# Kernel tuning notes

Hardware: AMD Instinct MI355X
Metric: run time of the kernel (lower is better)

The kernel has to match this reference:

```python
import jax, jax.numpy as jnp
import numpy as np

_J6 = jnp.array([[0,0,0,0,0,1],[0,0,0,0,-1,0],[0,0,0,1,0,0],
                 [0,0,1,0,0,0],[0,-1,0,0,0,0],[1,0,0,0,0,0]], dtype=jnp.float32)
_PAIRS4 = [(0,1),(0,2),(0,3),(1,2),(1,3),(2,3)]  # combinations(range(4),2)


def exterior(p1, p2):
    # Plucker line coords of two 4-vectors, normalized. (...,4)x(...,4)->(...,6)
    parts = [p1[..., i] * p2[..., j] - p1[..., j] * p2[..., i] for i, j in _PAIRS4]
    L = jnp.stack(parts, axis=-1)
    n = jnp.maximum(jnp.linalg.norm(L, axis=-1, keepdims=True), 1e-12)
    return L / n


def setup_inputs() -> dict:
    key = jax.random.key(0)
    B, T, D, H = 2, 2048, 1024, 16
    ks = jax.random.split(key, 10)
    w = lambda k, shape: jax.random.normal(k, shape, jnp.float32) * 0.02
    return {
        "x": jax.random.normal(ks[0], (B, T, D), jnp.float32),
        "qkv_w": w(ks[1], (3 * D, D)),
        "qkv_b": jnp.zeros((3 * D,), jnp.float32),
        "w1w": w(ks[2], (4 * H, D)),
        "w2w": w(ks[3], (4 * H, D)),
        "r1w": w(ks[4], (4 * H, D)),
        "r2w": w(ks[5], (4 * H, D)),
        "memv_w": w(ks[6], (D, D)),
        "memv_b": jnp.zeros((D,), jnp.float32),
        "memg_w": w(ks[7], (H, D)),
        "memg_b": jnp.zeros((H,), jnp.float32),
        "mem_scale": jnp.full((H,), 0.1, jnp.float32),
        "iter_mix": jnp.array(0.0, jnp.float32),
        "out_w": w(ks[8], (D, D)),
        "out_b": jnp.zeros((D,), jnp.float32),
        "decay_logits": jnp.full((H,), 4.6, jnp.float32),
    }


def reference(x, qkv_w, qkv_b, w1w, w2w, r1w, r2w, memv_w, memv_b,
              memg_w, memg_b, mem_scale, iter_mix, out_w, out_b, decay_logits):
    B, T, D = x.shape
    H = decay_logits.shape[0]
    dh = D // H
    pd = 6
    scale = dh ** -0.5

    # --- standard causal softmax attention ---
    qkv = (x @ qkv_w.T + qkv_b).reshape(B, T, 3, H, dh)
    qkv = jnp.transpose(qkv, (2, 0, 3, 1, 4))  # (3,B,H,T,dh)
    q, k, v = qkv[0], qkv[1], qkv[2]
    scores = jnp.einsum('bhtd,bhsd->bhts', q, k) * scale
    causal = jnp.triu(jnp.ones((T, T), dtype=bool), 1)
    scores = jnp.where(causal, -jnp.inf, scores)
    attn = jax.nn.softmax(scores, axis=-1)  # dropout is identity in eval
    seq_out = jnp.einsum('bhts,bhsd->bhtd', attn, v)
    seq_out = jnp.transpose(seq_out, (0, 2, 1, 3)).reshape(B, T, D)

    # --- decay-weighted Gram memory (linear-attention style state) ---
    x_prev = jnp.concatenate([jnp.zeros((B, 1, D), x.dtype), x[:, :-1]], axis=1)
    w1 = (x_prev @ w1w.T).reshape(B, T, H, 4)
    w2 = (x @ w2w.T).reshape(B, T, H, 4)
    write_lines = exterior(w1, w2)  # (B,T,H,6)
    r1 = (x @ r1w.T).reshape(B, T, H, 4)
    r2 = (x @ r2w.T).reshape(B, T, H, 4)
    read_lines = exterior(r1, r2)

    Jw = jnp.einsum('bthi,ij->bhtj', write_lines, _J6)  # (B,H,T,6)
    rd = jnp.transpose(read_lines, (0, 2, 1, 3))        # (B,H,T,6)

    decays = jax.nn.sigmoid(decay_logits)               # (H,)
    pos = jnp.arange(T, dtype=x.dtype)
    outer = Jw[..., :, None] * Jw[..., None, :]         # (B,H,T,6,6)
    decay_inv = (1.0 / jnp.maximum(decays, 1e-6))[:, None] ** pos[None, :]  # (H,T)
    outer_scaled = outer * decay_inv[None, :, :, None, None]
    M_cumsum = jnp.cumsum(outer_scaled, axis=2)
    M_cumsum = jnp.concatenate(
        [jnp.zeros((B, H, 1, pd, pd), x.dtype), M_cumsum[:, :, :-1]], axis=2)
    decay_fwd = decays[:, None] ** pos[None, :]
    M_all = M_cumsum * decay_fwd[None, :, :, None, None]

    rd_M = jnp.einsum('bhti,bhtij->bhtj', rd, M_all)
    score_M = jnp.sum(rd_M * rd, axis=-1)    # (B,H,T)
    score_M2 = jnp.sum(rd_M * rd_M, axis=-1)
    alpha = jax.nn.sigmoid(iter_mix)
    mem_score = (1 - alpha) * score_M + alpha * score_M2

    mem_val = x @ memv_w.T + memv_b                     # (B,T,D)
    gate = jax.nn.sigmoid(x @ memg_w.T + memg_b)        # (B,T,H)
    mem_score_t = jnp.transpose(mem_score, (0, 2, 1))   # (B,T,H)
    gated = jax.nn.sigmoid(mem_score_t * mem_scale) * gate
    gated = jnp.mean(gated, axis=-1, keepdims=True)     # (B,T,1)

    return (seq_out + gated * mem_val) @ out_w.T + out_b
```

## Files before the change

kernel.cpp:

```cpp
#include <hip/hip_runtime.h>
#include <stdint.h>

#define TT 2048
#define DD 1024
#define HH 16
#define LDP 4368
#define SCH 64
#define SNC (TT/SCH)

using bf16x8 = __attribute__((ext_vector_type(8))) __bf16;
using u16x8  = __attribute__((ext_vector_type(8))) unsigned short;
using f32x4  = __attribute__((ext_vector_type(4))) float;

__device__ __forceinline__ float bf2f(unsigned short u){
  unsigned int x = ((unsigned int)u) << 16;
  return __builtin_bit_cast(float, x);
}
__device__ __forceinline__ unsigned short f2bf(float f){
  unsigned int x = __builtin_bit_cast(unsigned int, f);
  x += 0x7fffu + ((x >> 16) & 1u);
  return (unsigned short)(x >> 16);
}
__device__ __forceinline__ float sigmoidf_(float x){ return 1.0f/(1.0f+__expf(-x)); }

__device__ __forceinline__ void gload_lds16(const void* g, void* l){
  auto gp = (const __attribute__((address_space(1))) unsigned int*)(uintptr_t)g;
  auto lp = (__attribute__((address_space(3))) unsigned int*)(unsigned int)(uintptr_t)l;
  __builtin_amdgcn_global_load_lds(gp, lp, 16, 0, 0);
}

__global__ void prep_all_kernel(const float* __restrict__ qkv_w, const float* __restrict__ w1w,
                                const float* __restrict__ w2w, const float* __restrict__ r1w,
                                const float* __restrict__ r2w, const float* __restrict__ memv_w,
                                const float* __restrict__ memg_w, const float* __restrict__ out_w,
                                const float* __restrict__ qkv_b, const float* __restrict__ memv_b,
                                const float* __restrict__ memg_b, const float* __restrict__ x,
                                unsigned short* __restrict__ Wcat, float* __restrict__ bcat,
                                unsigned short* __restrict__ xb)
{
  const int blk = blockIdx.x;
  if (blk < 5392) {
    const int idx = blk*256 + threadIdx.x;
    {
      const int row = idx >> 8, c4 = (idx & 255)*4;
      const float* src; int r;
      if      (row < 3072) { src = qkv_w;  r = row; }
      else if (row < 3136) { src = w1w;    r = row-3072; }
      else if (row < 3200) { src = w2w;    r = row-3136; }
      else if (row < 3264) { src = r1w;    r = row-3200; }
      else if (row < 3328) { src = r2w;    r = row-3264; }
      else if (row < 4352) { src = memv_w; r = row-3328; }
      else if (row < 4368) { src = memg_w; r = row-4352; }
      else                 { src = out_w;  r = row-4368; }
      const float4 v = *(const float4*)(src + (size_t)r*1024 + c4);
      ushort4 o; o.x=f2bf(v.x); o.y=f2bf(v.y); o.z=f2bf(v.z); o.w=f2bf(v.w);
      *(ushort4*)(Wcat + (size_t)row*1024 + c4) = o;
    }
    if (idx < 4368) {
      float v;
      if      (idx < 3072) v = qkv_b[idx];
      else if (idx < 3328) v = 0.f;
      else if (idx < 4352) v = memv_b[idx-3328];
      else                 v = memg_b[idx-4352];
      bcat[idx] = v;
    }
  } else {
    const int idx = (blk - 5392)*256 + threadIdx.x;
    const float4 v = ((const float4*)x)[idx];
    ushort4 o; o.x=f2bf(v.x); o.y=f2bf(v.y); o.z=f2bf(v.z); o.w=f2bf(v.w);
    ((ushort4*)xb)[idx] = o;
  }
}

template<bool OUTF32>
__global__ __launch_bounds__(256, 3)
void gemm_bt_kernel(const unsigned short* __restrict__ A, int lda,
                    const unsigned short* __restrict__ Bt, int ldb,
                    const float* __restrict__ bias,
                    void* __restrict__ Cout, int ldc, int N, int K,
                    unsigned short* __restrict__ VTout)
{
  __shared__ unsigned short smem[24576];
  const int tid = threadIdx.x;
  const int w = tid >> 6, lane = tid & 63;
  const int l15 = lane & 15, l4 = lane >> 4;
  const int m0 = blockIdx.x * 128;
  const int n0 = blockIdx.y * 128;
  const int wr = (w >> 1) * 64, wc = (w & 1) * 64;

  const f32x4 zero = {0.f,0.f,0.f,0.f};
  f32x4 acc[4][4];
#pragma unroll
  for (int i = 0; i < 4; ++i)
#pragma unroll
    for (int j = 0; j < 4; ++j) acc[i][j] = zero;

  const int srow = lane >> 2;
  const int k8   = (lane & 3) * 8;

  auto stage = [&](int k0, int buf) {
#pragma unroll
    for (int q = 0; q < 4; ++q) {
      const int c = q*4 + w;
      const int rloc = (c & 7)*16 + srow;
      if (c < 8) {
        gload_lds16(A + (size_t)(m0 + rloc)*lda + k0 + k8,
                    (char*)smem + buf*8192 + (c&7)*1024);
      } else {
        int nrow = n0 + rloc; if (nrow >= N) nrow = N - 1;
        gload_lds16(Bt + (size_t)nrow*ldb + k0 + k8,
                    (char*)smem + 24576 + buf*8192 + (c&7)*1024);
      }
    }
  };

  stage(0, 0);
  if (K > 32) stage(32, 1);

  int ti = 0;
  for (int k0 = 0; k0 < K; k0 += 32, ++ti) {
    if (k0 + 32 < K) { asm volatile("s_waitcnt vmcnt(4)" ::: "memory"); }
    else             { asm volatile("s_waitcnt vmcnt(0)" ::: "memory"); }
    __builtin_amdgcn_s_barrier();
    if (k0 + 64 < K) stage(k0 + 64, (ti + 2) % 3);

    const int cur = ti % 3;
    bf16x8 af[4], bfr[4];
#pragma unroll
    for (int i = 0; i < 4; ++i) {
      af[i]  = *reinterpret_cast<const bf16x8*>((const char*)smem + cur*8192
                 + (wr + i*16 + l15)*64 + l4*16);
      bfr[i] = *reinterpret_cast<const bf16x8*>((const char*)smem + 24576 + cur*8192
                 + (wc + i*16 + l15)*64 + l4*16);
    }
#pragma unroll
    for (int i = 0; i < 4; ++i)
#pragma unroll
      for (int j = 0; j < 4; ++j)
        acc[i][j] = __builtin_amdgcn_mfma_f32_16x16x32_bf16(af[i], bfr[j], acc[i][j], 0, 0, 0);
  }

  if (OUTF32) {
#pragma unroll
    for (int i = 0; i < 4; ++i) {
      const int rowb = m0 + wr + i*16 + l4*4;
#pragma unroll
      for (int j = 0; j < 4; ++j) {
        const int col = n0 + wc + j*16 + l15;
        if (col < N) {
          const float bv = bias ? bias[col] : 0.0f;
#pragma unroll
          for (int r = 0; r < 4; ++r)
            ((float*)Cout)[(size_t)(rowb + r)*ldc + col] = acc[i][j][r] + bv;
        }
      }
    }
  } else {
    __syncthreads();
    const bool isV = (VTout != nullptr) && (n0 >= 2048) && (n0 < 3072);
#pragma unroll
    for (int i = 0; i < 4; ++i) {
      const int rloc = wr + i*16 + l4*4;
#pragma unroll
      for (int j = 0; j < 4; ++j) {
        const int col = wc + j*16 + l15;
        const float bv = bias ? bias[n0 + col] : 0.0f;
#pragma unroll
        for (int r = 0; r < 4; ++r) {
          const int row = rloc + r;
          const unsigned byte = (unsigned)row*256u
                              + (((unsigned)col*2u) ^ (((unsigned)row & 15u) << 4));
          *(unsigned short*)((char*)smem + byte) = f2bf(acc[i][j][r] + bv);
        }
      }
    }
    __syncthreads();
    if (!isV) {
#pragma unroll
      for (int p = 0; p < 8; ++p) {
        const int idx = p*256 + tid;
        const int row = idx >> 4;
        const int c8  = (idx & 15) * 8;
        if (n0 + c8 + 8 <= N) {
          const unsigned byte = (unsigned)row*256u
                              + (((unsigned)(c8*2)) ^ (((unsigned)row & 15u) << 4));
          *(u16x8*)((unsigned short*)Cout + (size_t)(m0 + row)*ldc + n0 + c8) =
              *(const u16x8*)((const char*)smem + byte);
        }
      }
    } else {
      const int vbase = ((m0 >> 11)*HH + ((n0 - 2048) >> 6)) * 64;
      const int t0 = m0 & (TT - 1);
      for (int it = 0; it < 64; ++it) {
        const int i2 = it*256 + tid;
        const int d2 = i2 >> 7;
        const int tl = i2 & 127;
        const unsigned byte = (unsigned)tl*256u
                            + (((unsigned)d2*2u) ^ (((unsigned)tl & 15u) << 4));
        VTout[(size_t)(vbase + d2)*TT + t0 + tl] =
            *(const unsigned short*)((const char*)smem + byte);
      }
    }
  }
}

__global__ __launch_bounds__(256, 2)
void attn_kernel(const unsigned short* __restrict__ P,
                 const unsigned short* __restrict__ VT,
                 float* __restrict__ seqo)
{
  __shared__ unsigned short Ks[2][128*64];
  __shared__ unsigned short Vs[2][64*128];
  __shared__ unsigned short Pls[4][16*128];

  const int tid = threadIdx.x;
  const int w = tid >> 6, lane = tid & 63;
  const int l15 = lane & 15, l4 = lane >> 4;

  const int n = blockIdx.x;
  const int xcd = n & 7, slot = n >> 3;
  const int grp = slot >> 4, pi = slot & 15;
  const int g = grp*8 + xcd;
  const int h = g & 15, b = g >> 4;

  auto stage = [&](int kt, int bufsel) {
#pragma unroll
    for (int q2 = 0; q2 < 4; ++q2) {
      const int idx = q2*256 + tid;
      {
        const int r = idx >> 3;
        const int cb = ((idx & 7)*16) ^ ((r & 7) << 4);
        gload_lds16(P + (size_t)(b*TT + kt*128 + r)*LDP + 1024 + h*64 + (cb >> 1),
                    (char*)Ks[bufsel] + q2*4096 + w*1024);
      }
      {
        const int r = idx >> 4;
        const int cb = ((idx & 15)*16) ^ ((r & 7) << 4);
        gload_lds16(VT + (size_t)((b*HH + h)*64 + r)*TT + kt*128 + (cb >> 1),
                    (char*)Vs[bufsel] + q2*4096 + w*1024);
      }
    }
  };

  const f32x4 zero = {0.f,0.f,0.f,0.f};
  const unsigned xorb = ((unsigned)(l15 & 7u)) << 4;

  for (int rep = 0; rep < 2; ++rep) {
    const int qt = rep == 0 ? pi : 31 - pi;
    const int qbase = qt * 64;
    const int qrow = qbase + w*16 + l15;
    const int nt = (qt >> 1) + 1;

    bf16x8 qa[2];
    {
      const size_t base = (size_t)(b*TT + qbase + w*16 + l15)*LDP + h*64 + l4*8;
      qa[0] = *reinterpret_cast<const bf16x8*>(P + base);
      qa[1] = *reinterpret_cast<const bf16x8*>(P + base + 32);
    }

    f32x4 o[4];
#pragma unroll
    for (int d = 0; d < 4; ++d) o[d] = zero;
    float mrow = -1e30f;
    float lrow = 0.f;

    stage(0, 0);
    asm volatile("s_waitcnt vmcnt(0)" ::: "memory");
    __builtin_amdgcn_s_barrier();

    for (int kt = 0; kt < nt; ++kt) {
      const int cur = kt & 1;
      if (kt + 1 < nt) stage(kt + 1, cur ^ 1);

      f32x4 s[8];
#pragma unroll
      for (int kk = 0; kk < 8; ++kk) {
        f32x4 a = zero;
#pragma unroll
        for (int c = 0; c < 2; ++c) {
          const unsigned kbyte = (unsigned)((kk*16 + l15)*128)
                               + (((unsigned)(c*64 + l4*16)) ^ xorb);
          const bf16x8 kb = *reinterpret_cast<const bf16x8*>((const char*)Ks[cur] + kbyte);
          a = __builtin_amdgcn_mfma_f32_16x16x32_bf16(kb, qa[c], a, 0, 0, 0);
        }
        s[kk] = a;
      }

      if (kt == nt - 1) {
#pragma unroll
        for (int kk = 0; kk < 8; ++kk)
#pragma unroll
          for (int j = 0; j < 4; ++j) {
            const int kcol = kt*128 + kk*16 + l4*4 + j;
            s[kk][j] = (kcol <= qrow) ? s[kk][j]*0.125f : -1e30f;
          }
      } else {
#pragma unroll
        for (int kk = 0; kk < 8; ++kk)
#pragma unroll
          for (int j = 0; j < 4; ++j) s[kk][j] *= 0.125f;
      }

      float am[8];
#pragma unroll
      for (int kk = 0; kk < 8; ++kk)
        am[kk] = fmaxf(fmaxf(s[kk][0], s[kk][1]), fmaxf(s[kk][2], s[kk][3]));
      float tmax = fmaxf(fmaxf(fmaxf(am[0], am[1]), fmaxf(am[2], am[3])),
                         fmaxf(fmaxf(am[4], am[5]), fmaxf(am[6], am[7])));
      tmax = fmaxf(tmax, __shfl_xor(tmax, 16));
      tmax = fmaxf(tmax, __shfl_xor(tmax, 32));
      const bool skip = (__all(tmax <= mrow) != 0);
      const float mn = skip ? mrow : fmaxf(mrow, tmax);
      float lsum = 0.f;
#pragma unroll
      for (int kk = 0; kk < 8; ++kk) {
        float p0 = __expf(s[kk][0] - mn);
        float p1 = __expf(s[kk][1] - mn);
        float p2 = __expf(s[kk][2] - mn);
        float p3 = __expf(s[kk][3] - mn);
        s[kk][0] = p0; s[kk][1] = p1; s[kk][2] = p2; s[kk][3] = p3;
        lsum += (p0 + p1) + (p2 + p3);
      }
      lsum += __shfl_xor(lsum, 16);
      lsum += __shfl_xor(lsum, 32);

      if (skip) {
        lrow = lrow + lsum;
      } else {
        const float corr = __expf(mrow - mn);
        mrow = mn;
        lrow = lrow*corr + lsum;
        float corrq[4];
#pragma unroll
        for (int j = 0; j < 4; ++j) corrq[j] = __shfl(corr, l4*4 + j, 16);
#pragma unroll
        for (int d = 0; d < 4; ++d)
#pragma unroll
          for (int j = 0; j < 4; ++j) o[d][j] *= corrq[j];
      }

      const unsigned pbase = (unsigned)(w*4096);
#pragma unroll
      for (int kk = 0; kk < 8; ++kk)
#pragma unroll
        for (int jp = 0; jp < 2; ++jp) {
          const unsigned v = (unsigned)f2bf(s[kk][jp*2]) | ((unsigned)f2bf(s[kk][jp*2+1]) << 16);
          const unsigned k = (unsigned)(kk*16 + l4*4 + jp*2);
          unsigned byte = (unsigned)l15*256u + ((k*2u) ^ xorb);
          *(unsigned*)((char*)Pls + pbase + byte) = v;
        }
      asm volatile("s_waitcnt lgkmcnt(0)" ::: "memory");

#pragma unroll
      for (int c = 0; c < 4; ++c) {
        const unsigned abyte = (unsigned)(l15*256) + (((unsigned)(c*64 + l4*16)) ^ xorb);
        const bf16x8 pa = *reinterpret_cast<const bf16x8*>((char*)Pls + pbase + abyte);
#pragma unroll
        for (int d = 0; d < 4; ++d) {
          const unsigned vbyte = (unsigned)((d*16 + l15)*256)
                               + (((unsigned)(c*64 + l4*16)) ^ xorb);
          const bf16x8 vb = *reinterpret_cast<const bf16x8*>((const char*)Vs[cur] + vbyte);
          o[d] = __builtin_amdgcn_mfma_f32_16x16x32_bf16(pa, vb, o[d], 0, 0, 0);
        }
      }

      asm volatile("s_waitcnt lgkmcnt(0)" ::: "memory");
      asm volatile("s_waitcnt vmcnt(0)" ::: "memory");
      __builtin_amdgcn_s_barrier();
    }

    float lrowq[4];
#pragma unroll
    for (int j = 0; j < 4; ++j) lrowq[j] = __shfl(lrow, l4*4 + j, 16);
#pragma unroll
    for (int d = 0; d < 4; ++d)
#pragma unroll
      for (int j = 0; j < 4; ++j) {
        const int row = qbase + w*16 + l4*4 + j;
        seqo[(size_t)(b*TT + row)*DD + h*64 + d*16 + l15] = o[d][j] / lrowq[j];
      }
  }
}

__device__ __forceinline__ void ext6(const float* p, const float* q, float* L){
  L[0] = p[0]*q[1] - p[1]*q[0];
  L[1] = p[0]*q[2] - p[2]*q[0];
  L[2] = p[0]*q[3] - p[3]*q[0];
  L[3] = p[1]*q[2] - p[2]*q[1];
  L[4] = p[1]*q[3] - p[3]*q[1];
  L[5] = p[2]*q[3] - p[3]*q[2];
  const float n2 = L[0]*L[0]+L[1]*L[1]+L[2]*L[2]+L[3]*L[3]+L[4]*L[4]+L[5]*L[5];
  const float inv = 1.0f / fmaxf(sqrtf(n2), 1e-12f);
#pragma unroll
  for (int i = 0; i < 6; ++i) L[i] *= inv;
}

__device__ __forceinline__ void load4bf(const unsigned short* p, float* o){
  const ushort4 u = *(const ushort4*)p;
  o[0] = bf2f(u.x); o[1] = bf2f(u.y); o[2] = bf2f(u.z); o[3] = bf2f(u.w);
}

__global__ __launch_bounds__(64, 8)
void scan_passA(const unsigned short* __restrict__ P, const float* __restrict__ decay_logits,
                float* __restrict__ E)
{
  __shared__ float jwS[SCH][6];
  const int bid = blockIdx.x;
  const int s = bid >> 5, c = bid & (SNC-1);
  const int b_ = s >> 4, h = s & (HH-1);
  const int lane = threadIdx.x;

  {
    const int t = c*SCH + lane;
    const size_t row = (size_t)(b_*TT + t)*LDP;
    float w1[4], w2[4];
    if (t > 0) load4bf(P + row - LDP + 3072 + h*4, w1);
    else { w1[0]=w1[1]=w1[2]=w1[3]=0.f; }
    load4bf(P + row + 3136 + h*4, w2);
    float wl[6];
    ext6(w1, w2, wl);
    jwS[lane][0]= wl[5]; jwS[lane][1]=-wl[4]; jwS[lane][2]= wl[3];
    jwS[lane][3]= wl[2]; jwS[lane][4]=-wl[1]; jwS[lane][5]= wl[0];
  }
  __syncthreads();

  const int i = lane & 7, j = lane >> 3;
  const int ic = i < 6 ? i : 0, jc = j < 6 ? j : 0;
  const float d = sigmoidf_(decay_logits[h]);
  float e = 0.f;
  for (int t = 0; t < SCH; ++t)
    e = d*(e + jwS[t][ic]*jwS[t][jc]);
  if (i < 6 && j < 6) E[(size_t)bid*36 + j*6 + i] = e;
}

__global__ __launch_bounds__(64, 8)
void scan_passC(const unsigned short* __restrict__ P, const float* __restrict__ E,
                const float* __restrict__ decay_logits,
                const float* __restrict__ iter_mix, float* __restrict__ msc)
{
  __shared__ float Ls[SCH][12];
  const int bid = blockIdx.x;
  const int s = bid >> 5, c = bid & (SNC-1);
  const int b_ = s >> 4, h = s & (HH-1);
  const int lane = threadIdx.x;

  {
    const int t = c*SCH + lane;
    const size_t row = (size_t)(b_*TT + t)*LDP;
    float w1[4], w2[4], r1[4], r2[4];
    if (t > 0) load4bf(P + row - LDP + 3072 + h*4, w1);
    else { w1[0]=w1[1]=w1[2]=w1[3]=0.f; }
    load4bf(P + row + 3136 + h*4, w2);
    load4bf(P + row + 3200 + h*4, r1);
    load4bf(P + row + 3264 + h*4, r2);
    float wl[6], rl[6];
    ext6(w1, w2, wl);
    ext6(r1, r2, rl);
    Ls[lane][0]= wl[5]; Ls[lane][1]=-wl[4]; Ls[lane][2]= wl[3];
    Ls[lane][3]= wl[2]; Ls[lane][4]=-wl[1]; Ls[lane][5]= wl[0];
#pragma unroll
    for (int q = 0; q < 6; ++q) Ls[lane][6+q] = rl[q];
  }
  __syncthreads();

  const int i = lane & 7, j = lane >> 3;
  const bool valid = (i < 6) && (j < 6);
  const int ic = i < 6 ? i : 0, jc = j < 6 ? j : 0;
  const float d = sigmoidf_(decay_logits[h]);
  const float alpha = sigmoidf_(iter_mix[0]);

  float m = 0.f;
  if (valid) {
    const float dL = __powf(d, (float)SCH);
    for (int cp = 0; cp < c; ++cp)
      m = dL*m + E[((size_t)s*SNC + cp)*36 + j*6 + i];
  }

  for (int t = 0; t < SCH; ++t) {
    const float ai = Ls[t][ic];
    const float aj = Ls[t][jc];
    const float ri = Ls[t][6+ic];
    const float rj = Ls[t][6+jc];
    float part = valid ? ri*m : 0.f;
    part += __shfl_xor(part, 1);
    part += __shfl_xor(part, 2);
    part += __shfl_xor(part, 4);
    float contrib = (i == 0 && j < 6) ? part*((1.f-alpha)*rj + alpha*part) : 0.f;
    contrib += __shfl_xor(contrib, 8);
    contrib += __shfl_xor(contrib, 16);
    contrib += __shfl_xor(contrib, 32);
    if (lane == 0) msc[((size_t)b_*TT + c*SCH + t)*HH + h] = contrib;
    m = d*(m + ai*aj);
  }
}

__global__ __launch_bounds__(256, 4)
void combine_kernel(const float* __restrict__ seqo, const unsigned short* __restrict__ P,
                    const float* __restrict__ msc, const float* __restrict__ mem_scale,
                    unsigned short* __restrict__ zb)
{
  const int w = threadIdx.x >> 6, lane = threadIdx.x & 63;
  const int row = blockIdx.x*4 + w;
  float val = 0.f;
  if (lane < HH) {
    const float ms = msc[(size_t)row*HH + lane];
    const float gl = bf2f(P[(size_t)row*LDP + 4352 + lane]);
    val = sigmoidf_(ms*mem_scale[lane]) * sigmoidf_(gl);
  }
  val += __shfl_xor(val, 1);
  val += __shfl_xor(val, 2);
  val += __shfl_xor(val, 4);
  val += __shfl_xor(val, 8);
  const float g = __shfl(val, 0) * (1.0f/16.0f);
#pragma unroll
  for (int it = 0; it < 4; ++it) {
    const int dcol = it*256 + lane*4;
    const float4 sv = *(const float4*)&seqo[(size_t)row*DD + dcol];
    const ushort4 pv = *(const ushort4*)&P[(size_t)row*LDP + 3328 + dcol];
    ushort4 o;
    o.x = f2bf(sv.x + g*bf2f(pv.x));
    o.y = f2bf(sv.y + g*bf2f(pv.y));
    o.z = f2bf(sv.z + g*bf2f(pv.z));
    o.w = f2bf(sv.w + g*bf2f(pv.w));
    *(ushort4*)&zb[(size_t)row*DD + dcol] = o;
  }
}

extern "C" void kernel_launch(void* const* d_in, const int* in_sizes, int n_in,
                              void* d_out, int out_size, void* d_ws, size_t ws_size,
                              hipStream_t stream)
{
  const float* x            = (const float*)d_in[0];
  const float* qkv_w        = (const float*)d_in[1];
  const float* qkv_b        = (const float*)d_in[2];
  const float* w1w          = (const float*)d_in[3];
  const float* w2w          = (const float*)d_in[4];
  const float* r1w          = (const float*)d_in[5];
  const float* r2w          = (const float*)d_in[6];
  const float* memv_w       = (const float*)d_in[7];
  const float* memv_b       = (const float*)d_in[8];
  const float* memg_w       = (const float*)d_in[9];
  const float* memg_b       = (const float*)d_in[10];
  const float* mem_scale    = (const float*)d_in[11];
  const float* iter_mix     = (const float*)d_in[12];
  const float* out_w        = (const float*)d_in[13];
  const float* out_b        = (const float*)d_in[14];
  const float* decay_logits = (const float*)d_in[15];

  char* ws = (char*)d_ws;
  unsigned short* xb   = (unsigned short*)(ws + 0);
  unsigned short* Wcat = (unsigned short*)(ws + 8388608);
  float*          bcat = (float*)         (ws + 19431424);
  unsigned short* P    = (unsigned short*)(ws + 19449088);
  unsigned short* VT   = (unsigned short*)(ws + 55231744);
  float*          seqo = (float*)         (ws + 63620352);
  float*          E    = (float*)         (ws + 80397568);
  float*          msc  = (float*)         (ws + 83690752);
  unsigned short* zb   = xb;

  prep_all_kernel<<<9488, 256, 0, stream>>>(qkv_w, w1w, w2w, r1w, r2w, memv_w, memg_w, out_w,
                                            qkv_b, memv_b, memg_b, x, Wcat, bcat, xb);
  gemm_bt_kernel<false><<<dim3(32, 35), 256, 0, stream>>>(xb, 1024, Wcat, 1024, bcat,
                                                          P, LDP, 4368, 1024, VT);
  attn_kernel<<<512, 256, 0, stream>>>(P, VT, seqo);
  scan_passA<<<1024, 64, 0, stream>>>(P, decay_logits, E);
  scan_passC<<<1024, 64, 0, stream>>>(P, E, decay_logits, iter_mix, msc);
  combine_kernel<<<1024, 256, 0, stream>>>(seqo, P, msc, mem_scale, zb);
  gemm_bt_kernel<true><<<dim3(32, 8), 256, 0, stream>>>(zb, 1024, Wcat + (size_t)4368*1024, 1024,
                                                        out_b, d_out, 1024, 1024, 1024, nullptr);
}
```

Before: 171.2 us.

## Fold scan pass A into attention launch and store attention output as bf16

```diff
diff --git a/kernel.cpp b/kernel.cpp
--- a/kernel.cpp
+++ b/kernel.cpp
@@ -27,6 +27,24 @@
   auto gp = (const __attribute__((address_space(1))) unsigned int*)(uintptr_t)g;
   auto lp = (__attribute__((address_space(3))) unsigned int*)(unsigned int)(uintptr_t)l;
   __builtin_amdgcn_global_load_lds(gp, lp, 16, 0, 0);
+}
+
+__device__ __forceinline__ void ext6(const float* p, const float* q, float* L){
+  L[0] = p[0]*q[1] - p[1]*q[0];
+  L[1] = p[0]*q[2] - p[2]*q[0];
+  L[2] = p[0]*q[3] - p[3]*q[0];
+  L[3] = p[1]*q[2] - p[2]*q[1];
+  L[4] = p[1]*q[3] - p[3]*q[1];
+  L[5] = p[2]*q[3] - p[3]*q[2];
+  const float n2 = L[0]*L[0]+L[1]*L[1]+L[2]*L[2]+L[3]*L[3]+L[4]*L[4]+L[5]*L[5];
+  const float inv = 1.0f / fmaxf(sqrtf(n2), 1e-12f);
+#pragma unroll
+  for (int i = 0; i < 6; ++i) L[i] *= inv;
+}
+
+__device__ __forceinline__ void load4bf(const unsigned short* p, float* o){
+  const ushort4 u = *(const ushort4*)p;
+  o[0] = bf2f(u.x); o[1] = bf2f(u.y); o[2] = bf2f(u.z); o[3] = bf2f(u.w);
 }
 
 __global__ void prep_all_kernel(const float* __restrict__ qkv_w, const float* __restrict__ w1w,
@@ -207,7 +225,9 @@
 __global__ __launch_bounds__(256, 2)
 void attn_kernel(const unsigned short* __restrict__ P,
                  const unsigned short* __restrict__ VT,
-                 float* __restrict__ seqo)
+                 unsigned short* __restrict__ seqo,
+                 const float* __restrict__ decay_logits,
+                 float* __restrict__ E)
 {
   __shared__ unsigned short Ks[2][128*64];
   __shared__ unsigned short Vs[2][64*128];
@@ -216,6 +236,35 @@
   const int tid = threadIdx.x;
   const int w = tid >> 6, lane = tid & 63;
   const int l15 = lane & 15, l4 = lane >> 4;
+
+  if (blockIdx.x >= 512) {
+    float* jwS = (float*)Ks + (size_t)w * SCH * 6;
+    const int chunk = (blockIdx.x - 512)*4 + w;
+    const int s = chunk >> 5, c = chunk & (SNC-1);
+    const int b_ = s >> 4, h = s & (HH-1);
+    {
+      const int t = c*SCH + lane;
+      const size_t row = (size_t)(b_*TT + t)*LDP;
+      float w1[4], w2[4];
+      if (t > 0) load4bf(P + row - LDP + 3072 + h*4, w1);
+      else { w1[0]=w1[1]=w1[2]=w1[3]=0.f; }
+      load4bf(P + row + 3136 + h*4, w2);
+      float wl[6];
+      ext6(w1, w2, wl);
+      jwS[lane*6+0]= wl[5]; jwS[lane*6+1]=-wl[4]; jwS[lane*6+2]= wl[3];
+      jwS[lane*6+3]= wl[2]; jwS[lane*6+4]=-wl[1]; jwS[lane*6+5]= wl[0];
+    }
+    asm volatile("s_waitcnt lgkmcnt(0)" ::: "memory");
+
+    const int i = lane & 7, j = lane >> 3;
+    const int ic = i < 6 ? i : 0, jc = j < 6 ? j : 0;
+    const float d = sigmoidf_(decay_logits[h]);
+    float e = 0.f;
+    for (int t = 0; t < SCH; ++t)
+      e = d*(e + jwS[t*6+ic]*jwS[t*6+jc]);
+    if (i < 6 && j < 6) E[(size_t)chunk*36 + j*6 + i] = e;
+    return;
+  }
 
   const int n = blockIdx.x;
   const int xcd = n & 7, slot = n >> 3;
@@ -377,60 +426,9 @@
 #pragma unroll
       for (int j = 0; j < 4; ++j) {
         const int row = qbase + w*16 + l4*4 + j;
-        seqo[(size_t)(b*TT + row)*DD + h*64 + d*16 + l15] = o[d][j] / lrowq[j];
-      }
-  }
-}
-
-__device__ __forceinline__ void ext6(const float* p, const float* q, float* L){
-  L[0] = p[0]*q[1] - p[1]*q[0];
-  L[1] = p[0]*q[2] - p[2]*q[0];
-  L[2] = p[0]*q[3] - p[3]*q[0];
-  L[3] = p[1]*q[2] - p[2]*q[1];
-  L[4] = p[1]*q[3] - p[3]*q[1];
-  L[5] = p[2]*q[3] - p[3]*q[2];
-  const float n2 = L[0]*L[0]+L[1]*L[1]+L[2]*L[2]+L[3]*L[3]+L[4]*L[4]+L[5]*L[5];
-  const float inv = 1.0f / fmaxf(sqrtf(n2), 1e-12f);
-#pragma unroll
-  for (int i = 0; i < 6; ++i) L[i] *= inv;
-}
-
-__device__ __forceinline__ void load4bf(const unsigned short* p, float* o){
-  const ushort4 u = *(const ushort4*)p;
-  o[0] = bf2f(u.x); o[1] = bf2f(u.y); o[2] = bf2f(u.z); o[3] = bf2f(u.w);
-}
-
-__global__ __launch_bounds__(64, 8)
-void scan_passA(const unsigned short* __restrict__ P, const float* __restrict__ decay_logits,
-                float* __restrict__ E)
-{
-  __shared__ float jwS[SCH][6];
-  const int bid = blockIdx.x;
-  const int s = bid >> 5, c = bid & (SNC-1);
-  const int b_ = s >> 4, h = s & (HH-1);
-  const int lane = threadIdx.x;
-
-  {
-    const int t = c*SCH + lane;
-    const size_t row = (size_t)(b_*TT + t)*LDP;
-    float w1[4], w2[4];
-    if (t > 0) load4bf(P + row - LDP + 3072 + h*4, w1);
-    else { w1[0]=w1[1]=w1[2]=w1[3]=0.f; }
-    load4bf(P + row + 3136 + h*4, w2);
-    float wl[6];
-    ext6(w1, w2, wl);
-    jwS[lane][0]= wl[5]; jwS[lane][1]=-wl[4]; jwS[lane][2]= wl[3];
-    jwS[lane][3]= wl[2]; jwS[lane][4]=-wl[1]; jwS[lane][5]= wl[0];
-  }
-  __syncthreads();
-
-  const int i = lane & 7, j = lane >> 3;
-  const int ic = i < 6 ? i : 0, jc = j < 6 ? j : 0;
-  const float d = sigmoidf_(decay_logits[h]);
-  float e = 0.f;
-  for (int t = 0; t < SCH; ++t)
-    e = d*(e + jwS[t][ic]*jwS[t][jc]);
-  if (i < 6 && j < 6) E[(size_t)bid*36 + j*6 + i] = e;
+        seqo[(size_t)(b*TT + row)*DD + h*64 + d*16 + l15] = f2bf(o[d][j] / lrowq[j]);
+      }
+  }
 }
 
 __global__ __launch_bounds__(64, 8)
@@ -495,7 +493,7 @@
 }
 
 __global__ __launch_bounds__(256, 4)
-void combine_kernel(const float* __restrict__ seqo, const unsigned short* __restrict__ P,
+void combine_kernel(const unsigned short* __restrict__ seqo, const unsigned short* __restrict__ P,
                     const float* __restrict__ msc, const float* __restrict__ mem_scale,
                     unsigned short* __restrict__ zb)
 {
@@ -515,13 +513,13 @@
 #pragma unroll
   for (int it = 0; it < 4; ++it) {
     const int dcol = it*256 + lane*4;
-    const float4 sv = *(const float4*)&seqo[(size_t)row*DD + dcol];
+    const ushort4 sv = *(const ushort4*)&seqo[(size_t)row*DD + dcol];
     const ushort4 pv = *(const ushort4*)&P[(size_t)row*LDP + 3328 + dcol];
     ushort4 o;
-    o.x = f2bf(sv.x + g*bf2f(pv.x));
-    o.y = f2bf(sv.y + g*bf2f(pv.y));
-    o.z = f2bf(sv.z + g*bf2f(pv.z));
-    o.w = f2bf(sv.w + g*bf2f(pv.w));
+    o.x = f2bf(bf2f(sv.x) + g*bf2f(pv.x));
+    o.y = f2bf(bf2f(sv.y) + g*bf2f(pv.y));
+    o.z = f2bf(bf2f(sv.z) + g*bf2f(pv.z));
+    o.w = f2bf(bf2f(sv.w) + g*bf2f(pv.w));
     *(ushort4*)&zb[(size_t)row*DD + dcol] = o;
   }
 }
@@ -553,7 +551,7 @@
   float*          bcat = (float*)         (ws + 19431424);
   unsigned short* P    = (unsigned short*)(ws + 19449088);
   unsigned short* VT   = (unsigned short*)(ws + 55231744);
-  float*          seqo = (float*)         (ws + 63620352);
+  unsigned short* seqo = (unsigned short*)(ws + 63620352);
   float*          E    = (float*)         (ws + 80397568);
   float*          msc  = (float*)         (ws + 83690752);
   unsigned short* zb   = xb;
@@ -562,8 +560,7 @@
                                             qkv_b, memv_b, memg_b, x, Wcat, bcat, xb);
   gemm_bt_kernel<false><<<dim3(32, 35), 256, 0, stream>>>(xb, 1024, Wcat, 1024, bcat,
                                                           P, LDP, 4368, 1024, VT);
-  attn_kernel<<<512, 256, 0, stream>>>(P, VT, seqo);
-  scan_passA<<<1024, 64, 0, stream>>>(P, decay_logits, E);
+  attn_kernel<<<768, 256, 0, stream>>>(P, VT, seqo, decay_logits, E);
   scan_passC<<<1024, 64, 0, stream>>>(P, E, decay_logits, iter_mix, msc);
   combine_kernel<<<1024, 256, 0, stream>>>(seqo, P, msc, mem_scale, zb);
   gemm_bt_kernel<true><<<dim3(32, 8), 256, 0, stream>>>(zb, 1024, Wcat + (size_t)4368*1024, 1024,
```

Measured after the change: 166.2 us (median of 2 runs). 1.03x faster.
